# Performance work log

Measured on AMD Instinct MI355X. Metric: run time of the kernel, lower is better.

The kernel has to match this reference:

```python
import math
import jax, jax.numpy as jnp
import numpy as np

N_HEADS = 16
D_HEAD = 128
D_ROPE = 64  # d_head // 2
ROPE_SCALE = 40.0


def _rotate_half(x):
    x1, x2 = jnp.split(x, 2, axis=-1)
    return jnp.concatenate([-x2, x1], axis=-1)


def _apply_rotary(x, cos, sin):
    # rotate only the first cos.shape[-1] dims of the rope slice
    half = cos.shape[-1]
    x_rot, x_base = x[..., :half], x[..., half:]
    x_rot = x_rot * cos + _rotate_half(x_rot) * sin
    return jnp.concatenate([x_rot, x_base], axis=-1)


def _forward(x, W_dkv, W_dq, W_uk, W_uv, W_uq, W_kr, W_qr, W_out):
    B, S, H = x.shape
    c_kv = x @ W_dkv                                   # [B,S,cd]
    c_q = x @ W_dq                                     # [B,S,cd]
    q_c = c_q @ W_uq                                   # [B,S,up]
    k_c = c_kv @ W_uk                                  # [B,S,up]
    v = (c_kv @ W_uv).reshape(B, S, N_HEADS, D_HEAD)   # [B,S,h,d]
    k_r = (x @ W_kr).reshape(B, S, N_HEADS, D_ROPE)
    q_r = (q_c @ W_qr).reshape(B, S, N_HEADS, D_ROPE)

    # RoPE (partial: first d_rope//2 dims rotated, rest passthrough)
    half_dim = D_ROPE // 2
    inv_freq = 1.0 / (10000.0 ** (jnp.arange(0, half_dim, 2, dtype=jnp.float32) / half_dim))
    t = jnp.arange(S, dtype=jnp.float32) / ROPE_SCALE
    freqs = jnp.einsum('i,j->ij', t, inv_freq)         # [S, d_rope//4]
    rotation = jnp.concatenate([freqs, freqs], axis=-1)  # [S, d_rope//2]
    cos = jnp.cos(rotation)[None, :, None, :]
    sin = jnp.sin(rotation)[None, :, None, :]
    k_rope = _apply_rotary(k_r, cos, sin)
    q_rope = _apply_rotary(q_r, cos, sin)

    k = jnp.concatenate([k_c.reshape(B, S, N_HEADS, D_HEAD - D_ROPE), k_rope], axis=-1)
    q = jnp.concatenate([q_c.reshape(B, S, N_HEADS, D_HEAD - D_ROPE), q_rope], axis=-1)

    # NOTE: faithful to source: einsum takes (k, q) in that order, and the
    # softmax result is computed but UNUSED (AV uses raw scores). Replicated.
    scores = jnp.einsum('bihd,bjhd->bhij', k, q) / math.sqrt(D_HEAD)
    out = jnp.einsum('bhij,bjhd->bihd', scores, v)     # [B,S,h,d]
    output = out.reshape(B, S, N_HEADS * D_HEAD) @ W_out
    return output, c_kv, k_rope


def setup_inputs() -> dict:
    key = jax.random.key(0)
    ks = jax.random.split(key, 9)
    B, S, H, CD, UP = 2, 2048, 2048, 1024, 1024
    w = lambda k, shp: jax.random.normal(k, shp, dtype=jnp.float32) * 0.02
    return {
        'x': jax.random.normal(ks[0], (B, S, H), dtype=jnp.float32),
        'W_dkv': w(ks[1], (H, CD)),
        'W_dq': w(ks[2], (H, CD)),
        'W_uk': w(ks[3], (CD, UP)),
        'W_uv': w(ks[4], (CD, N_HEADS * D_HEAD)),
        'W_uq': w(ks[5], (CD, UP)),
        'W_kr': w(ks[6], (H, N_HEADS * D_ROPE)),
        'W_qr': w(ks[7], (CD, N_HEADS * D_ROPE)),
        'W_out': w(ks[8], (N_HEADS * D_HEAD, H)),
    }


def reference(x, W_dkv, W_dq, W_uk, W_uv, W_uq, W_kr, W_qr, W_out):
    return _forward(x, W_dkv, W_dq, W_uk, W_uv, W_uq, W_kr, W_qr, W_out)
```

## Files before the change

kernel.cpp:

```cpp
#include <hip/hip_runtime.h>
#include <math.h>

typedef _Float16 half8 __attribute__((ext_vector_type(8)));
typedef float floatx4 __attribute__((ext_vector_type(4)));

typedef const uint32_t __attribute__((address_space(1)))* gp1_t;
typedef uint32_t __attribute__((address_space(3)))* lp3_t;
#define GLDS16(g, l) __builtin_amdgcn_global_load_lds((gp1_t)(const void*)(g), (lp3_t)(void*)(l), 16, 0, 0)

#define BK 32

#define BARRIER() __builtin_amdgcn_s_barrier()
#define VM3()     asm volatile("s_waitcnt vmcnt(3)" ::: "memory")

__device__ inline int xcd_swz(int wg, int nwg)
{
    int q = nwg >> 3, r = nwg & 7;
    int xcd = wg & 7, idx = wg >> 3;
    return (xcd < r) ? (xcd * (q + 1) + idx) : (r * (q + 1) + (xcd - r) * q + idx);
}

__global__ __launch_bounds__(256) void gemm_fast(
    const _Float16* __restrict__ A, const _Float16* __restrict__ B,
    float* __restrict__ Cf, _Float16* __restrict__ Ch,
    float* __restrict__ Cx, _Float16* __restrict__ Cy,
    int Kc, long lda, long ldb, long ldcf, long ldch,
    int cmap, long cf_lo, long cf_hi, float alpha, int nh, int nsk, int epi_mode,
    long aoff_b, long aoff_h, long boff_b, long boff_h,
    long coff_b, long coff_h, long coff_s)
{
    __shared__ __align__(16) _Float16 As[128 * BK];
    __shared__ __align__(16) _Float16 Bs[128 * BK];

    const int z = blockIdx.z;
    const int hs = nh * nsk;
    const int zb = z / hs;
    const int rr = z % hs;
    const int zh = rr / nsk;
    const int ks = rr % nsk;

    const _Float16* Ab = A + (long)zb * aoff_b + (long)zh * aoff_h + (long)ks * Kc;
    const _Float16* Bb = B + (long)zb * boff_b + (long)zh * boff_h + (long)ks * Kc;
    const long cofs = (long)zb * coff_b + (long)zh * coff_h + (long)ks * coff_s;

    const int nwg = gridDim.x * gridDim.y;
    const int swz = xcd_swz(blockIdx.y * gridDim.x + blockIdx.x, nwg);
    const long m0 = (long)(swz / gridDim.x) * 128;
    const long n0 = (long)(swz % gridDim.x) * 128;
    const int t = threadIdx.x;
    const int wave = t >> 6, lane = t & 63;
    const int lr = lane & 15, lq = lane >> 4;
    const int wm = (wave & 1) * 64, wn = (wave >> 1) * 64;

    const int c0 = wave * 64 + lane;
    const int c1 = c0 + 256;
    const _Float16* ga0 = Ab + (m0 + (c0 >> 2)) * lda + (c0 & 3) * 8;
    const _Float16* ga1 = Ab + (m0 + (c1 >> 2)) * lda + (c1 & 3) * 8;
    const _Float16* gb0 = Bb + (n0 + (c0 >> 2)) * ldb + (c0 & 3) * 8;
    const _Float16* gb1 = Bb + (n0 + (c1 >> 2)) * ldb + (c1 & 3) * 8;
    _Float16* lA0 = As + wave * 512;
    _Float16* lA1 = As + 2048 + wave * 512;
    _Float16* lB0 = Bs + wave * 512;
    _Float16* lB1 = Bs + 2048 + wave * 512;

    floatx4 acc[4][4];
    #pragma unroll
    for (int i = 0; i < 4; ++i)
        #pragma unroll
        for (int j = 0; j < 4; ++j) acc[i][j] = (floatx4){0.f, 0.f, 0.f, 0.f};

    for (int k0 = 0; k0 < Kc; k0 += BK) {
        GLDS16(ga0, lA0); GLDS16(ga1, lA1);
        GLDS16(gb0, lB0); GLDS16(gb1, lB1);
        ga0 += BK; ga1 += BK; gb0 += BK; gb1 += BK;
        __syncthreads();

        half8 a[4], b[4];
        #pragma unroll
        for (int i = 0; i < 4; ++i) a[i] = *(const half8*)(As + (wm + i * 16 + lr) * BK + lq * 8);
        #pragma unroll
        for (int j = 0; j < 4; ++j) b[j] = *(const half8*)(Bs + (wn + j * 16 + lr) * BK + lq * 8);
        #pragma unroll
        for (int i = 0; i < 4; ++i)
            #pragma unroll
            for (int j = 0; j < 4; ++j)
                acc[i][j] = __builtin_amdgcn_mfma_f32_16x16x32_f16(a[i], b[j], acc[i][j], 0, 0, 0);
        __syncthreads();
    }

    if (epi_mode == 0) {
        #pragma unroll
        for (int i = 0; i < 4; ++i)
            #pragma unroll
            for (int j = 0; j < 4; ++j)
                #pragma unroll
                for (int r = 0; r < 4; ++r) {
                    long row = m0 + wm + i * 16 + lq * 4 + r;
                    long col = n0 + wn + j * 16 + lr;
                    float v = alpha * acc[i][j][r];
                    if (Ch) {
                        long cm = cmap ? ((col >> 6) * 128 + (col & 63)) : col;
                        Ch[cofs + row * ldch + cm] = (_Float16)v;
                    }
                    if (Cf && col >= cf_lo && col < cf_hi)
                        Cf[cofs + row * ldcf + (col - cf_lo)] = v;
                }
    } else if (epi_mode == 1) {
        const int nb = (int)n0 + wn;
        if (nb < 2048) {
            #pragma unroll
            for (int i = 0; i < 4; ++i)
                #pragma unroll
                for (int j = 0; j < 4; ++j)
                    #pragma unroll
                    for (int r = 0; r < 4; ++r) {
                        long row = m0 + wm + i * 16 + lq * 4 + r;
                        long col = n0 + wn + j * 16 + lr;
                        float v = acc[i][j][r];
                        Ch[row * 2048 + col] = (_Float16)v;
                        if (nb < 1024) Cf[row * 1024 + col] = v;
                    }
        } else {
            const int h = (nb - 2048) >> 6;
            const float invf = powf(10000.0f, -(float)lr / 16.0f);
            #pragma unroll
            for (int i = 0; i < 4; ++i)
                #pragma unroll
                for (int r = 0; r < 4; ++r) {
                    long row = m0 + wm + i * 16 + lq * 4 + r;
                    int s = (int)row & 2047;
                    float ang = ((float)s / 40.0f) * invf;
                    float cv = cosf(ang), sv = sinf(ang);
                    float v0 = acc[i][0][r], v1 = acc[i][1][r];
                    float y[4] = { v0 * cv - v1 * sv, v1 * cv + v0 * sv,
                                   acc[i][2][r], acc[i][3][r] };
                    #pragma unroll
                    for (int j = 0; j < 4; ++j) {
                        int d = j * 16 + lr;
                        Cx[row * 1024 + h * 64 + d] = y[j];
                        Cy[row * 2048 + h * 128 + 64 + d] = (_Float16)y[j];
                    }
                }
        }
    } else {
        if (zb == 0) {
            #pragma unroll
            for (int i = 0; i < 4; ++i)
                #pragma unroll
                for (int j = 0; j < 4; ++j)
                    #pragma unroll
                    for (int r = 0; r < 4; ++r) {
                        long row = m0 + wm + i * 16 + lq * 4 + r;
                        long col = n0 + wn + j * 16 + lr;
                        Ch[cofs + row * ldch + col] = (_Float16)acc[i][j][r];
                    }
        } else {
            const int mb = (int)m0 + wm;
            if (mb < 1024) {
                #pragma unroll
                for (int i = 0; i < 4; ++i)
                    #pragma unroll
                    for (int j = 0; j < 4; ++j)
                        #pragma unroll
                        for (int r = 0; r < 4; ++r) {
                            long u = m0 + wm + i * 16 + lq * 4 + r;
                            long col = n0 + wn + j * 16 + lr;
                            long qrow = ((u >> 6) << 7) + (u & 63);
                            Ch[cofs + qrow * 4096 + col] = (_Float16)acc[i][j][r];
                        }
            } else {
                const int h = (mb - 1024) >> 6;
                #pragma unroll
                for (int j = 0; j < 4; ++j)
                    #pragma unroll
                    for (int r = 0; r < 4; ++r) {
                        long col = n0 + wn + j * 16 + lr;
                        int s = (int)col & 2047;
                        int j16 = lq * 4 + r;
                        float ivf = powf(10000.0f, -(float)j16 / 16.0f);
                        float ang = ((float)s / 40.0f) * ivf;
                        float cv = cosf(ang), sv = sinf(ang);
                        float v0 = acc[0][j][r], v1 = acc[1][j][r];
                        float y[4] = { v0 * cv - v1 * sv, v1 * cv + v0 * sv,
                                       acc[2][j][r], acc[3][j][r] };
                        #pragma unroll
                        for (int i = 0; i < 4; ++i) {
                            int dd = i * 16 + lq * 4 + r;
                            long qrow = h * 128 + 64 + dd;
                            Ch[cofs + qrow * 4096 + col] = (_Float16)y[i];
                        }
                    }
            }
        }
    }
}

__global__ __launch_bounds__(512, 4) void gemm256(
    const _Float16* __restrict__ A, const _Float16* __restrict__ B,
    float* __restrict__ Cf, _Float16* __restrict__ Ch,
    float* __restrict__ Cx, _Float16* __restrict__ Cy,
    int Kc, long lda, long ldb, long ldcf, long ldch,
    int cmap, long cf_lo, long cf_hi, float alpha, int nh, int nsk, int epi_mode,
    long aoff_b, long aoff_h, long boff_b, long boff_h,
    long coff_b, long coff_h, long coff_s)
{
    __shared__ __align__(16) _Float16 sm[36864];

    const int z = blockIdx.z;
    const int hs = nh * nsk;
    const int zb = z / hs;
    const int rr = z % hs;
    const int zh = rr / nsk;
    const int ks = rr % nsk;

    const _Float16* Ab = A + (long)zb * aoff_b + (long)zh * aoff_h + (long)ks * Kc;
    const _Float16* Bb = B + (long)zb * boff_b + (long)zh * boff_h + (long)ks * Kc;
    const long cofs = (long)zb * coff_b + (long)zh * coff_h + (long)ks * coff_s;

    const int nwg = gridDim.x * gridDim.y;
    const int swz = xcd_swz(blockIdx.y * gridDim.x + blockIdx.x, nwg);
    const long m0 = (long)(swz / gridDim.x) * 256;
    const long n0 = (long)(swz % gridDim.x) * 128;
    const int t = threadIdx.x;
    const int wave = t >> 6, lane = t & 63;
    const int lr = lane & 15, lq = lane >> 4;
    const int wm = (wave >> 1) * 64, wn = (wave & 1) * 64;
    const int wmrb = (wave >> 1) * 4, wnrb = (wave & 1) * 4;
    const int NT = Kc >> 5;

    floatx4 acc[4][4];
    #pragma unroll
    for (int i = 0; i < 4; ++i)
        #pragma unroll
        for (int j = 0; j < 4; ++j) acc[i][j] = (floatx4){0.f, 0.f, 0.f, 0.f};

#define ST(tt_, q_, sl_) do { \
        const int tcl_ = (tt_) < NT ? (tt_) : (tt_) - NT; \
        const int isB_ = ((q_) == 2); \
        const int u_ = isB_ ? wave : wave * 2 + (q_); \
        const long grow_ = (isB_ ? n0 : m0) + u_ * 16 + lr; \
        const _Float16* src_ = (isB_ ? Bb + grow_ * ldb : Ab + grow_ * lda) \
                               + (long)tcl_ * 32 + lq * 8; \
        _Float16* dst_ = sm + (sl_) * 12288 + (isB_ ? 8192 : 0) + u_ * 512; \
        GLDS16(src_, dst_); \
    } while (0)

#define LOADA(sl_) { _Pragma("unroll") \
    for (int i_ = 0; i_ < 4; ++i_) \
        aF[i_] = *(const half8*)(sm + (sl_) * 12288 + (wmrb + i_) * 512 + lane * 8); }
#define LOADB(sl_) { _Pragma("unroll") \
    for (int j_ = 0; j_ < 4; ++j_) \
        bF[j_] = *(const half8*)(sm + (sl_) * 12288 + 8192 + (wnrb + j_) * 512 + lane * 8); }
#define MFMA16() { _Pragma("unroll") \
    for (int i_ = 0; i_ < 4; ++i_) { _Pragma("unroll") \
        for (int j_ = 0; j_ < 4; ++j_) \
            acc[i_][j_] = __builtin_amdgcn_mfma_f32_16x16x32_f16(aF[i_], bF[j_], acc[i_][j_], 0, 0, 0); } }

    ST(0, 0, 0); ST(0, 1, 0); ST(0, 2, 0);
    ST(1, 0, 1); ST(1, 1, 1); ST(1, 2, 1);
    VM3(); BARRIER();

    half8 aF[4], bF[4];
    int sc = 0, ss = 2;
    for (int tt = 0; tt < NT; ++tt) {
        ST(tt + 2, 0, ss); ST(tt + 2, 1, ss); ST(tt + 2, 2, ss);
        LOADA(sc); LOADB(sc);
        __builtin_amdgcn_s_setprio(1); MFMA16(); __builtin_amdgcn_s_setprio(0);
        VM3();
        BARRIER();
        sc = (sc == 2) ? 0 : sc + 1;
        ss = (ss == 2) ? 0 : ss + 1;
    }
#undef ST
#undef LOADA
#undef LOADB
#undef MFMA16

    if (epi_mode == 0) {
        #pragma unroll
        for (int i = 0; i < 4; ++i)
            #pragma unroll
            for (int j = 0; j < 4; ++j)
                #pragma unroll
                for (int r = 0; r < 4; ++r) {
                    long row = m0 + wm + i * 16 + lq * 4 + r;
                    long col = n0 + wn + j * 16 + lr;
                    float v = alpha * acc[i][j][r];
                    if (Ch) {
                        long cm = cmap ? ((col >> 6) * 128 + (col & 63)) : col;
                        Ch[cofs + row * ldch + cm] = (_Float16)v;
                    }
                    if (Cf && col >= cf_lo && col < cf_hi)
                        Cf[cofs + row * ldcf + (col - cf_lo)] = v;
                }
    } else if (epi_mode == 1) {
        const int nb = (int)n0 + wn;
        if (nb < 2048) {
            #pragma unroll
            for (int i = 0; i < 4; ++i)
                #pragma unroll
                for (int j = 0; j < 4; ++j)
                    #pragma unroll
                    for (int r = 0; r < 4; ++r) {
                        long row = m0 + wm + i * 16 + lq * 4 + r;
                        long col = n0 + wn + j * 16 + lr;
                        float v = acc[i][j][r];
                        Ch[row * 2048 + col] = (_Float16)v;
                        if (nb < 1024) Cf[row * 1024 + col] = v;
                    }
        } else {
            const int h = (nb - 2048) >> 6;
            const float invf = powf(10000.0f, -(float)lr / 16.0f);
            #pragma unroll
            for (int i = 0; i < 4; ++i)
                #pragma unroll
                for (int r = 0; r < 4; ++r) {
                    long row = m0 + wm + i * 16 + lq * 4 + r;
                    int s = (int)row & 2047;
                    float ang = ((float)s / 40.0f) * invf;
                    float cv = cosf(ang), sv = sinf(ang);
                    float v0 = acc[i][0][r], v1 = acc[i][1][r];
                    float y[4] = { v0 * cv - v1 * sv, v1 * cv + v0 * sv,
                                   acc[i][2][r], acc[i][3][r] };
                    #pragma unroll
                    for (int j = 0; j < 4; ++j) {
                        int d = j * 16 + lr;
                        Cx[row * 1024 + h * 64 + d] = y[j];
                        Cy[row * 2048 + h * 128 + 64 + d] = (_Float16)y[j];
                    }
                }
        }
    } else {
        if (zb == 0) {
            #pragma unroll
            for (int i = 0; i < 4; ++i)
                #pragma unroll
                for (int j = 0; j < 4; ++j)
                    #pragma unroll
                    for (int r = 0; r < 4; ++r) {
                        long row = m0 + wm + i * 16 + lq * 4 + r;
                        long col = n0 + wn + j * 16 + lr;
                        Ch[cofs + row * ldch + col] = (_Float16)acc[i][j][r];
                    }
        } else {
            const int mb = (int)m0 + wm;
            if (mb < 1024) {
                #pragma unroll
                for (int i = 0; i < 4; ++i)
                    #pragma unroll
                    for (int j = 0; j < 4; ++j)
                        #pragma unroll
                        for (int r = 0; r < 4; ++r) {
                            long u = m0 + wm + i * 16 + lq * 4 + r;
                            long col = n0 + wn + j * 16 + lr;
                            long qrow = ((u >> 6) << 7) + (u & 63);
                            Ch[cofs + qrow * 4096 + col] = (_Float16)acc[i][j][r];
                        }
            } else {
                const int h = (mb - 1024) >> 6;
                #pragma unroll
                for (int j = 0; j < 4; ++j)
                    #pragma unroll
                    for (int r = 0; r < 4; ++r) {
                        long col = n0 + wn + j * 16 + lr;
                        int s = (int)col & 2047;
                        int j16 = lq * 4 + r;
                        float ivf = powf(10000.0f, -(float)j16 / 16.0f);
                        float ang = ((float)s / 40.0f) * ivf;
                        float cv = cosf(ang), sv = sinf(ang);
                        float v0 = acc[0][j][r], v1 = acc[1][j][r];
                        float y[4] = { v0 * cv - v1 * sv, v1 * cv + v0 * sv,
                                       acc[2][j][r], acc[3][j][r] };
                        #pragma unroll
                        for (int i = 0; i < 4; ++i) {
                            int dd = i * 16 + lq * 4 + r;
                            long qrow = h * 128 + 64 + dd;
                            Ch[cofs + qrow * 4096 + col] = (_Float16)y[i];
                        }
                    }
            }
        }
    }
}

__device__ inline void tr_tile(const float* __restrict__ in, _Float16* __restrict__ out,
                               int R, int C, int tile, int tx, int ty, float (*tb)[33])
{
    int tc = tile % (C >> 5), tr = tile / (C >> 5);
    int c0 = tc * 32, r0 = tr * 32;
    for (int i = ty; i < 32; i += 8)
        tb[i][tx] = in[(long)(r0 + i) * C + c0 + tx];
    __syncthreads();
    for (int i = ty; i < 32; i += 8)
        out[(long)(c0 + i) * R + r0 + tx] = (_Float16)tb[tx][i];
}

__device__ inline void cast_blk(const float* __restrict__ in, _Float16* __restrict__ out,
                                int blk, int tid)
{
    long idx = (long)blk * 2048 + tid * 8;
    float4 a = ((const float4*)(in + idx))[0];
    float4 b = ((const float4*)(in + idx))[1];
    half8 h = { (_Float16)a.x, (_Float16)a.y, (_Float16)a.z, (_Float16)a.w,
                (_Float16)b.x, (_Float16)b.y, (_Float16)b.z, (_Float16)b.w };
    *(half8*)(out + idx) = h;
}

__global__ void prep_kernel(
    const float* __restrict__ x, const float* __restrict__ W_dkv,
    const float* __restrict__ W_dq, const float* __restrict__ W_uk,
    const float* __restrict__ W_uv, const float* __restrict__ W_uq,
    const float* __restrict__ W_kr, const float* __restrict__ W_qr,
    const float* __restrict__ W_out,
    _Float16* __restrict__ WcatT, _Float16* __restrict__ WukT,
    _Float16* __restrict__ WuvT, _Float16* __restrict__ WuqcatT,
    _Float16* __restrict__ WqrT, _Float16* __restrict__ Wuqh,
    _Float16* __restrict__ WoutT, _Float16* __restrict__ xh)
{
    __shared__ float tb[32][33];
    int blk = blockIdx.x;
    int tid = threadIdx.x;
    int tx = tid & 31, ty = tid >> 5;
    if (blk < 2048)        tr_tile(W_dkv, WcatT,            2048, 1024, blk,         tx, ty, tb);
    else if (blk < 4096)   tr_tile(W_dq,  WcatT + 2097152,  2048, 1024, blk - 2048,  tx, ty, tb);
    else if (blk < 6144)   tr_tile(W_kr,  WcatT + 4194304,  2048, 1024, blk - 4096,  tx, ty, tb);
    else if (blk < 7168)   tr_tile(W_uk,  WukT,             1024, 1024, blk - 6144,  tx, ty, tb);
    else if (blk < 8192)   tr_tile(W_uq,  WuqcatT,          1024, 1024, blk - 7168,  tx, ty, tb);
    else if (blk < 9216)   tr_tile(W_qr,  WqrT,             1024, 1024, blk - 8192,  tx, ty, tb);
    else if (blk < 11264)  tr_tile(W_uv,  WuvT,             1024, 2048, blk - 9216,  tx, ty, tb);
    else if (blk < 15360)  tr_tile(W_out, WoutT,            2048, 2048, blk - 11264, tx, ty, tb);
    else if (blk < 19456)  cast_blk(x,    xh,   blk - 15360, tid);
    else                   cast_blk(W_uq, Wuqh, blk - 19456, tid);
}

__global__ void reduce8_cast_kernel(const float* __restrict__ in, _Float16* __restrict__ out)
{
    int i = blockIdx.x * 256 + threadIdx.x;
    float s = 0.f;
    #pragma unroll
    for (int j = 0; j < 8; ++j) s += in[i + j * 524288];
    out[i] = (_Float16)s;
}

extern "C" void kernel_launch(void* const* d_in, const int* in_sizes, int n_in,
                              void* d_out, int out_size, void* d_ws, size_t ws_size,
                              hipStream_t stream)
{
    const float* x     = (const float*)d_in[0];
    const float* W_dkv = (const float*)d_in[1];
    const float* W_dq  = (const float*)d_in[2];
    const float* W_uk  = (const float*)d_in[3];
    const float* W_uv  = (const float*)d_in[4];
    const float* W_uq  = (const float*)d_in[5];
    const float* W_kr  = (const float*)d_in[6];
    const float* W_qr  = (const float*)d_in[7];
    const float* W_out = (const float*)d_in[8];

    float* out_main  = (float*)d_out;
    float* out_ckv   = out_main + 8388608;
    float* out_krope = out_ckv + 4194304;

    char* w = (char*)d_ws;
    size_t off = 0;
    auto alloc = [&](size_t bytes) { void* p = w + off; off += (bytes + 255) & ~(size_t)255; return p; };

    _Float16* catA    = (_Float16*)alloc(16777216);
    _Float16* WcatT   = (_Float16*)alloc(12582912);
    _Float16* WukT    = (_Float16*)alloc(2097152);
    _Float16* WuvT    = (_Float16*)alloc(4194304);
    _Float16* WuqcatT = (_Float16*)alloc(4194304);
    _Float16* WqrT    = (_Float16*)alloc(2097152);
    _Float16* Wuqh    = (_Float16*)alloc(2097152);
    _Float16* WoutT   = (_Float16*)alloc(8388608);
    void*     reg_xm  = alloc(16777216);
    _Float16* k_flat  = (_Float16*)alloc(16777216);
    _Float16* vT      = (_Float16*)alloc(16777216);
    _Float16* qT      = (_Float16*)alloc(16777216);

    _Float16* xh      = (_Float16*)reg_xm;
    float*    Mbuf32p = (float*)reg_xm;
    _Float16* PT      = catA;
    _Float16* WuqrT   = WuqcatT + 1048576;
    _Float16* Mbuf16  = WukT;

    #define GF(A_,B_,Cf_,Ch_,Cx_,Cy_,M_,N_,Kc_,lda_,ldb_,ldcf_,ldch_,cmap_,cflo_,cfhi_,alpha_,nb_,nh_,nsk_,mode_,ab,ah,bb,bh,cb,ch2,cs) \
        hipLaunchKernelGGL(gemm_fast, dim3((N_)/128,(M_)/128,(nb_)*(nh_)*(nsk_)), dim3(256), 0, stream, \
            A_, B_, Cf_, Ch_, Cx_, Cy_, (int)(Kc_), (long)(lda_), (long)(ldb_), (long)(ldcf_), (long)(ldch_), \
            cmap_, (long)(cflo_), (long)(cfhi_), (float)(alpha_), nh_, nsk_, mode_, \
            (long)(ab),(long)(ah),(long)(bb),(long)(bh),(long)(cb),(long)(ch2),(long)(cs))

    #define GF256(A_,B_,Cf_,Ch_,Cx_,Cy_,M_,N_,Kc_,lda_,ldb_,ldcf_,ldch_,cmap_,cflo_,cfhi_,alpha_,nb_,nh_,nsk_,mode_,ab,ah,bb,bh,cb,ch2,cs) \
        hipLaunchKernelGGL(gemm256, dim3((N_)/128,(M_)/256,(nb_)*(nh_)*(nsk_)), dim3(512), 0, stream, \
            A_, B_, Cf_, Ch_, Cx_, Cy_, (int)(Kc_), (long)(lda_), (long)(ldb_), (long)(ldcf_), (long)(ldch_), \
            cmap_, (long)(cflo_), (long)(cfhi_), (float)(alpha_), nh_, nsk_, mode_, \
            (long)(ab),(long)(ah),(long)(bb),(long)(bh),(long)(cb),(long)(ch2),(long)(cs))

    hipLaunchKernelGGL(prep_kernel, dim3(19968), dim3(256), 0, stream,
        x, W_dkv, W_dq, W_uk, W_uv, W_uq, W_kr, W_qr, W_out,
        WcatT, WukT, WuvT, WuqcatT, WqrT, Wuqh, WoutT, xh);

    GF256(xh, WcatT, out_ckv, catA, out_krope, k_flat, 4096, 3072, 2048, 2048, 2048, 0, 0,
       0, 0, 0, 1.0, 1, 1, 1, 1, 0,0,0,0,0,0,0);
    GF(WqrT, Wuqh, (float*)nullptr, WuqrT, (float*)nullptr, (_Float16*)nullptr,
       1024, 1024, 1024, 1024, 1024, 0, 1024, 0, 0, 0, 1.0, 1, 1, 1, 0, 0,0,0,0,0,0,0);
    GF(catA, WukT, (float*)nullptr, k_flat, (float*)nullptr, (_Float16*)nullptr,
       4096, 1024, 1024, 2048, 1024, 0, 2048, 1, 0, 0, 1.0, 1, 1, 1, 0, 0,0,0,0,0,0,0);
    GF256(WuvT, catA, (float*)nullptr, vT, (float*)nullptr, (_Float16*)nullptr,
       2048, 4096, 1024, 1024, 2048, 0, 4096, 0, 0, 0, 1.0, 2, 1, 1, 2,
       2097152, 0, 1024, 0, 8388608, 0, 0);
    GF(qT, vT, Mbuf32p, (_Float16*)nullptr, (float*)nullptr, (_Float16*)nullptr,
       128, 128, 256, 4096, 4096, 128, 0, 0, 0, 128, 0.08838834764831845, 2, 16, 8, 0,
       2048, 524288, 2048, 524288, 262144, 16384, 524288);
    hipLaunchKernelGGL(reduce8_cast_kernel, dim3(2048), dim3(256), 0, stream, Mbuf32p, Mbuf16);
    GF(WoutT, Mbuf16, (float*)nullptr, PT, (float*)nullptr, (_Float16*)nullptr,
       2048, 128, 128, 2048, 128, 0, 2048, 0, 0, 0, 1.0, 2, 16, 1, 0,
       0, 128, 262144, 16384, 4194304, 128, 0);
    GF(k_flat, PT, out_main, (_Float16*)nullptr, (float*)nullptr, (_Float16*)nullptr,
       2048, 2048, 2048, 2048, 2048, 2048, 0, 0, 0, 2048, 1.0, 2, 1, 1, 0,
       4194304, 0, 4194304, 0, 4194304, 0, 0);

    #undef GF
    #undef GF256
}
```

Baseline: 464.3 us.

## Merge independent GEMMs into shared gemm256 launches via z-split dispatch

```diff
diff --git a/kernel.cpp b/kernel.cpp
--- a/kernel.cpp
+++ b/kernel.cpp
@@ -202,25 +202,43 @@
     int Kc, long lda, long ldb, long ldcf, long ldch,
     int cmap, long cf_lo, long cf_hi, float alpha, int nh, int nsk, int epi_mode,
     long aoff_b, long aoff_h, long boff_b, long boff_h,
-    long coff_b, long coff_h, long coff_s)
+    long coff_b, long coff_h, long coff_s,
+    int zsplit, int pgy,
+    const _Float16* __restrict__ A2, const _Float16* __restrict__ B2,
+    _Float16* __restrict__ Ch2,
+    int Kc2, long lda2, long ldb2, long ldch2, int mlim2, int nlim2, int cmap2)
 {
     __shared__ __align__(16) _Float16 sm[36864];
 
     const int z = blockIdx.z;
-    const int hs = nh * nsk;
-    const int zb = z / hs;
-    const int rr = z % hs;
-    const int zh = rr / nsk;
-    const int ks = rr % nsk;
-
-    const _Float16* Ab = A + (long)zb * aoff_b + (long)zh * aoff_h + (long)ks * Kc;
-    const _Float16* Bb = B + (long)zb * boff_b + (long)zh * boff_h + (long)ks * Kc;
-    const long cofs = (long)zb * coff_b + (long)zh * coff_h + (long)ks * coff_s;
-
-    const int nwg = gridDim.x * gridDim.y;
-    const int swz = xcd_swz(blockIdx.y * gridDim.x + blockIdx.x, nwg);
-    const long m0 = (long)(swz / gridDim.x) * 256;
-    const long n0 = (long)(swz % gridDim.x) * 128;
+    int zbv = 0;
+    long m0, n0, cofs = 0;
+    const _Float16 *Ab, *Bb;
+
+    if (z >= zsplit) {
+        if ((int)blockIdx.x >= nlim2 || (int)blockIdx.y >= mlim2) return;
+        Ab = A2; Bb = B2;
+        Kc = Kc2; lda = lda2; ldb = ldb2;
+        Ch = Ch2; ldch = ldch2; Cf = nullptr;
+        cmap = cmap2; alpha = 1.0f; epi_mode = 0;
+        m0 = (long)blockIdx.y * 256;
+        n0 = (long)blockIdx.x * 128;
+    } else {
+        if ((int)blockIdx.y >= pgy) return;
+        const int hs = nh * nsk;
+        zbv = z / hs;
+        const int rr = z % hs;
+        const int zh = rr / nsk;
+        const int ks = rr % nsk;
+        Ab = A + (long)zbv * aoff_b + (long)zh * aoff_h + (long)ks * Kc;
+        Bb = B + (long)zbv * boff_b + (long)zh * boff_h + (long)ks * Kc;
+        cofs = (long)zbv * coff_b + (long)zh * coff_h + (long)ks * coff_s;
+        const int nwg = gridDim.x * pgy;
+        const int swz = xcd_swz((int)blockIdx.y * gridDim.x + blockIdx.x, nwg);
+        m0 = (long)(swz / gridDim.x) * 256;
+        n0 = (long)(swz % gridDim.x) * 128;
+    }
+
     const int t = threadIdx.x;
     const int wave = t >> 6, lane = t & 63;
     const int lr = lane & 15, lq = lane >> 4;
@@ -331,7 +349,7 @@
                 }
         }
     } else {
-        if (zb == 0) {
+        if (zbv == 0) {
             #pragma unroll
             for (int i = 0; i < 4; ++i)
                 #pragma unroll
@@ -489,25 +507,26 @@
             cmap_, (long)(cflo_), (long)(cfhi_), (float)(alpha_), nh_, nsk_, mode_, \
             (long)(ab),(long)(ah),(long)(bb),(long)(bh),(long)(cb),(long)(ch2),(long)(cs))
 
-    #define GF256(A_,B_,Cf_,Ch_,Cx_,Cy_,M_,N_,Kc_,lda_,ldb_,ldcf_,ldch_,cmap_,cflo_,cfhi_,alpha_,nb_,nh_,nsk_,mode_,ab,ah,bb,bh,cb,ch2,cs) \
-        hipLaunchKernelGGL(gemm256, dim3((N_)/128,(M_)/256,(nb_)*(nh_)*(nsk_)), dim3(512), 0, stream, \
-            A_, B_, Cf_, Ch_, Cx_, Cy_, (int)(Kc_), (long)(lda_), (long)(ldb_), (long)(ldcf_), (long)(ldch_), \
-            cmap_, (long)(cflo_), (long)(cfhi_), (float)(alpha_), nh_, nsk_, mode_, \
-            (long)(ab),(long)(ah),(long)(bb),(long)(bh),(long)(cb),(long)(ch2),(long)(cs))
-
     hipLaunchKernelGGL(prep_kernel, dim3(19968), dim3(256), 0, stream,
         x, W_dkv, W_dq, W_uk, W_uv, W_uq, W_kr, W_qr, W_out,
         WcatT, WukT, WuvT, WuqcatT, WqrT, Wuqh, WoutT, xh);
 
-    GF256(xh, WcatT, out_ckv, catA, out_krope, k_flat, 4096, 3072, 2048, 2048, 2048, 0, 0,
-       0, 0, 0, 1.0, 1, 1, 1, 1, 0,0,0,0,0,0,0);
-    GF(WqrT, Wuqh, (float*)nullptr, WuqrT, (float*)nullptr, (_Float16*)nullptr,
-       1024, 1024, 1024, 1024, 1024, 0, 1024, 0, 0, 0, 1.0, 1, 1, 1, 0, 0,0,0,0,0,0,0);
-    GF(catA, WukT, (float*)nullptr, k_flat, (float*)nullptr, (_Float16*)nullptr,
-       4096, 1024, 1024, 2048, 1024, 0, 2048, 1, 0, 0, 1.0, 1, 1, 1, 0, 0,0,0,0,0,0,0);
-    GF256(WuvT, catA, (float*)nullptr, vT, (float*)nullptr, (_Float16*)nullptr,
-       2048, 4096, 1024, 1024, 2048, 0, 4096, 0, 0, 0, 1.0, 2, 1, 1, 2,
-       2097152, 0, 1024, 0, 8388608, 0, 0);
+    hipLaunchKernelGGL(gemm256, dim3(24, 16, 2), dim3(512), 0, stream,
+        xh, WcatT, out_ckv, catA, out_krope, k_flat,
+        2048, (long)2048, (long)2048, (long)0, (long)0,
+        0, (long)0, (long)0, 1.0f, 1, 1, 1,
+        (long)0, (long)0, (long)0, (long)0, (long)0, (long)0, (long)0,
+        1 , 16 ,
+        WqrT, Wuqh, WuqrT, 1024, (long)1024, (long)1024, (long)1024, 4, 8, 0);
+
+    hipLaunchKernelGGL(gemm256, dim3(32, 16, 3), dim3(512), 0, stream,
+        WuvT, catA, (float*)nullptr, vT, (float*)nullptr, (_Float16*)nullptr,
+        1024, (long)1024, (long)2048, (long)0, (long)4096,
+        0, (long)0, (long)0, 1.0f, 1, 1, 2,
+        (long)2097152, (long)0, (long)1024, (long)0, (long)8388608, (long)0, (long)0,
+        2 , 8 ,
+        catA, WukT, k_flat, 1024, (long)2048, (long)1024, (long)2048, 16, 8, 1);
+
     GF(qT, vT, Mbuf32p, (_Float16*)nullptr, (float*)nullptr, (_Float16*)nullptr,
        128, 128, 256, 4096, 4096, 128, 0, 0, 0, 128, 0.08838834764831845, 2, 16, 8, 0,
        2048, 524288, 2048, 524288, 262144, 16384, 524288);
@@ -520,5 +539,4 @@
        4194304, 0, 4194304, 0, 4194304, 0, 0);
 
     #undef GF
-    #undef GF256
-}
+}
```

After: 451.9 us. 2.7% less time.
